# Kernel tuning notes

Measured on AMD Instinct MI355X. Metric: run time of the kernel, lower is better.

The kernel has to match this reference:

```python
import math
import jax, jax.numpy as jnp
import numpy as np

NUM_BUCKETS = 32
MAX_DISTANCE = 128
N_HEADS = 16
D_KV = 64


def _relative_position_bucket(rel_pos, num_buckets=NUM_BUCKETS, max_distance=MAX_DISTANCE):
    # bidirectional=True branch of T5's bucketing
    num_buckets = num_buckets // 2
    rel_buckets = (rel_pos > 0).astype(jnp.int32) * num_buckets
    rel_pos = jnp.abs(rel_pos)
    max_exact = num_buckets // 2
    is_small = rel_pos < max_exact
    # safe log (values < max_exact are masked out by is_small)
    rp_f = jnp.maximum(rel_pos, 1).astype(jnp.float32)
    rel_if_large = max_exact + (
        jnp.log(rp_f / max_exact) / math.log(max_distance / max_exact) * (num_buckets - max_exact)
    ).astype(jnp.int32)
    rel_if_large = jnp.minimum(rel_if_large, num_buckets - 1)
    return rel_buckets + jnp.where(is_small, rel_pos, rel_if_large)


def compute_bias(rel_bias_table, q_len, k_len):
    ctx = jnp.arange(q_len)[:, None]
    mem = jnp.arange(k_len)[None, :]
    buckets = _relative_position_bucket(mem - ctx)  # [q, k]
    values = rel_bias_table[buckets]                # [q, k, h]
    return jnp.transpose(values, (2, 0, 1))[None]   # [1, h, q, k]


def setup_inputs() -> dict:
    key = jax.random.key(0)
    k1, k2, k3, k4 = jax.random.split(key, 4)
    d_model = 1024
    return {
        "hidden_states": jax.random.normal(k1, (2, 2048, d_model), jnp.float32),
        "w_qkv": jax.random.normal(k2, (d_model, 3 * N_HEADS * D_KV), jnp.float32) * (d_model ** -0.5),
        "w_o": jax.random.normal(k3, (N_HEADS * D_KV, d_model), jnp.float32) * ((N_HEADS * D_KV) ** -0.5),
        "rel_bias_table": jax.random.normal(k4, (NUM_BUCKETS, N_HEADS), jnp.float32),
    }


def reference(hidden_states, w_qkv, w_o, rel_bias_table):
    b, s, _ = hidden_states.shape
    inner = N_HEADS * D_KV
    qkv = hidden_states @ w_qkv                         # [b, s, 3*inner]
    q, k, v = jnp.split(qkv, [inner, 2 * inner], axis=-1)
    def to_bhsd(x):
        return jnp.transpose(x.reshape(b, s, N_HEADS, D_KV), (0, 2, 1, 3))
    q, k, v = to_bhsd(q), to_bhsd(k), to_bhsd(v)
    scores = jnp.einsum("bhqd,bhkd->bhqk", q, k)        # no 1/sqrt(d) scaling in T5
    position_bias = compute_bias(rel_bias_table, s, s)  # [1, h, q, k]
    scores = scores + position_bias
    attn = jax.nn.softmax(scores.astype(jnp.float32), axis=-1).astype(scores.dtype)
    out = jnp.einsum("bhqk,bhkd->bhqd", attn, v)
    out = jnp.transpose(out, (0, 2, 1, 3)).reshape(b, s, inner)
    attn_output = out @ w_o
    return attn_output, position_bias
```

## Files before the change

kernel.cpp:

```cpp
#include <hip/hip_runtime.h>
#include <hip/hip_bf16.h>
#include <cstdint>
#include <cstddef>

#define S_LEN 2048
#define NH 16
#define DKV 64
#define BATCH 2
#define DMODEL 1024

typedef _Float16 half_t;
typedef __attribute__((ext_vector_type(4))) _Float16 halfx4;
typedef __attribute__((ext_vector_type(8))) _Float16 half8;
typedef __attribute__((ext_vector_type(4))) float floatx4;

__device__ __forceinline__ void load_lds16(const half_t* g, half_t* l) {
  __builtin_amdgcn_global_load_lds((const __attribute__((address_space(1))) void*)g,
                                   (__attribute__((address_space(3))) void*)l, 16, 0, 0);
}

__device__ __forceinline__ int t5_bucket(int delta) {
  int base = (delta > 0) ? 16 : 0;
  int a = delta < 0 ? -delta : delta;
  int n;
  if (a < 8)       n = a;
  else if (a < 12) n = 8;
  else if (a < 16) n = 9;
  else if (a < 23) n = 10;
  else if (a < 32) n = 11;
  else if (a < 46) n = 12;
  else if (a < 64) n = 13;
  else if (a < 91) n = 14;
  else             n = 15;
  return base + n;
}

__global__ __launch_bounds__(256) void bias_kernel(const float* __restrict__ table,
                                                   float* __restrict__ out) {
  int h = blockIdx.x >> 11;
  int q = blockIdx.x & (S_LEN - 1);
  __shared__ float tb[32];
  if (threadIdx.x < 32) tb[threadIdx.x] = table[threadIdx.x * NH + h];
  __syncthreads();
  float* dst = out + (size_t)blockIdx.x * S_LEN;
  int k0 = threadIdx.x * 4;
#pragma unroll
  for (int half = 0; half < 2; half++) {
    int k = k0 + half * 1024;
    float4 v;
    v.x = tb[t5_bucket((k + 0) - q)];
    v.y = tb[t5_bucket((k + 1) - q)];
    v.z = tb[t5_bucket((k + 2) - q)];
    v.w = tb[t5_bucket((k + 3) - q)];
    *(float4*)(dst + k) = v;
  }
}

__global__ __launch_bounds__(256) void cast_f2h(const float* __restrict__ in,
                                                half_t* __restrict__ out) {
  int i = blockIdx.x * 256 + threadIdx.x;
  float4 v = ((const float4*)in)[i];
  halfx4 h;
  h[0] = (half_t)v.x; h[1] = (half_t)v.y; h[2] = (half_t)v.z; h[3] = (half_t)v.w;
  ((halfx4*)out)[i] = h;
}

__global__ __launch_bounds__(256) void transpose_cast(const float* __restrict__ in,
                                                      half_t* __restrict__ out,
                                                      int R, int C) {
  __shared__ float t[32][33];
  int lr = threadIdx.x >> 3;
  int lc = (threadIdx.x & 7) * 4;
  int r0 = blockIdx.y * 32, c0 = blockIdx.x * 32;
  float4 v = *(const float4*)(in + (size_t)(r0 + lr) * C + c0 + lc);
  t[lr][lc + 0] = v.x; t[lr][lc + 1] = v.y; t[lr][lc + 2] = v.z; t[lr][lc + 3] = v.w;
  __syncthreads();
  halfx4 hv;
#pragma unroll
  for (int u = 0; u < 4; u++) hv[u] = (half_t)t[lc + u][lr];
  *(halfx4*)(out + (size_t)(c0 + lr) * R + r0 + lc) = hv;
}

template <int MODE>
__global__ __launch_bounds__(256) void hgemm128(const half_t* __restrict__ A,
                                                const half_t* __restrict__ Bt,
                                                float* __restrict__ C,
                                                half_t* __restrict__ Qo,
                                                half_t* __restrict__ Ko,
                                                half_t* __restrict__ Vto,
                                                int M, int N, int K) {
  __shared__ half_t Asl[8 * 512];
  __shared__ half_t Bsl[8 * 512];

  const int tid = threadIdx.x;
  const int w = tid >> 6;
  const int lane = tid & 63;
  const int l15 = lane & 15;
  const int quad = lane >> 4;
  const int wm = w >> 1, wn = w & 1;
  const int m0 = blockIdx.y * 128;
  const int n0 = blockIdx.x * 128;

  floatx4 acc[4][4];
#pragma unroll
  for (int i = 0; i < 4; i++)
#pragma unroll
    for (int j = 0; j < 4; j++) acc[i][j] = (floatx4){0.f, 0.f, 0.f, 0.f};

  const half_t* ga0 = A + (size_t)(m0 + (2 * w + 0) * 16 + l15) * K + quad * 8;
  const half_t* ga1 = A + (size_t)(m0 + (2 * w + 1) * 16 + l15) * K + quad * 8;
  const half_t* gb0 = Bt + (size_t)(n0 + (2 * w + 0) * 16 + l15) * K + quad * 8;
  const half_t* gb1 = Bt + (size_t)(n0 + (2 * w + 1) * 16 + l15) * K + quad * 8;
  half_t* la0 = &Asl[(2 * w + 0) * 512];
  half_t* la1 = &Asl[(2 * w + 1) * 512];
  half_t* lb0 = &Bsl[(2 * w + 0) * 512];
  half_t* lb1 = &Bsl[(2 * w + 1) * 512];

  for (int k0 = 0; k0 < K; k0 += 32) {
    __syncthreads();
    load_lds16(ga0 + k0, la0);
    load_lds16(ga1 + k0, la1);
    load_lds16(gb0 + k0, lb0);
    load_lds16(gb1 + k0, lb1);
    __syncthreads();

    half8 af[4], bf[4];
#pragma unroll
    for (int i = 0; i < 4; i++) af[i] = *(half8*)&Asl[(wm * 4 + i) * 512 + lane * 8];
#pragma unroll
    for (int j = 0; j < 4; j++) bf[j] = *(half8*)&Bsl[(wn * 4 + j) * 512 + lane * 8];
#pragma unroll
    for (int i = 0; i < 4; i++)
#pragma unroll
      for (int j = 0; j < 4; j++)
        acc[i][j] = __builtin_amdgcn_mfma_f32_16x16x32_f16(af[i], bf[j], acc[i][j], 0, 0, 0);
  }

  const int rowbase = m0 + wm * 64;
  const int colbase = n0 + wn * 64;
  if (MODE == 0) {
#pragma unroll
    for (int i = 0; i < 4; i++)
#pragma unroll
      for (int j = 0; j < 4; j++)
#pragma unroll
        for (int r = 0; r < 4; r++)
          C[(size_t)(rowbase + i * 16 + quad * 4 + r) * N + colbase + j * 16 + l15] =
              acc[i][j][r];
  } else {
    const int which = colbase >> 10;
    const int h = (colbase & 1023) >> 6;
    const int b = rowbase >> 11;
    const int s0 = rowbase & (S_LEN - 1);
    if (which < 2) {
      half_t* base = ((which == 0) ? Qo : Ko) + (size_t)(b * NH + h) * S_LEN * DKV;
#pragma unroll
      for (int i = 0; i < 4; i++)
#pragma unroll
        for (int j = 0; j < 4; j++)
#pragma unroll
          for (int r = 0; r < 4; r++)
            base[(size_t)(s0 + i * 16 + quad * 4 + r) * DKV + j * 16 + l15] =
                (half_t)acc[i][j][r];
    } else {
      half_t* base = Vto + (size_t)(b * NH + h) * DKV * S_LEN;
#pragma unroll
      for (int i = 0; i < 4; i++)
#pragma unroll
        for (int j = 0; j < 4; j++)
#pragma unroll
          for (int r = 0; r < 4; r++)
            base[(size_t)(j * 16 + l15) * S_LEN + s0 + i * 16 + quad * 4 + r] =
                (half_t)acc[i][j][r];
    }
  }
}

__global__ __launch_bounds__(256) void attn_mfma(const half_t* __restrict__ Q,
                                                 const half_t* __restrict__ K,
                                                 const half_t* __restrict__ Vt,
                                                 const float* __restrict__ table,
                                                 half_t* __restrict__ X) {
  __shared__ half_t Ks[64 * 64];
  __shared__ half_t Vts[64 * 64];
  __shared__ half_t Ps[64 * 68];
  __shared__ float tb[32];

  const int tid = threadIdx.x;
  const int w = tid >> 6;
  const int lane = tid & 63;
  const int l15 = lane & 15;
  const int quad = lane >> 4;
  const int bh = blockIdx.y;
  const int h = bh & (NH - 1);
  const int b = bh >> 4;
  const int q0 = blockIdx.x * 64;

  if (tid < 32) tb[tid] = table[tid * NH + h];

  half8 qf[2];
#pragma unroll
  for (int ks = 0; ks < 2; ks++)
    qf[ks] = *(const half8*)(Q + ((size_t)bh * S_LEN + q0 + w * 16 + l15) * DKV +
                             ks * 32 + quad * 8);

  floatx4 o[4];
  float m[4], l[4];
#pragma unroll
  for (int r = 0; r < 4; r++) { m[r] = -1e30f; l[r] = 0.0f; }
#pragma unroll
  for (int nb = 0; nb < 4; nb++) o[nb] = (floatx4){0.f, 0.f, 0.f, 0.f};

  const int jr = tid >> 2;
  const int ub = (tid & 3) * 2;

  for (int kc = 0; kc < S_LEN; kc += 64) {
    __syncthreads();
    {
      const half_t* Kg = K + ((size_t)bh * S_LEN + kc + jr) * DKV + ub * 8;
      const half_t* Vg = Vt + ((size_t)bh * DKV + jr) * S_LEN + kc + ub * 8;
      half8 k0v = *(const half8*)(Kg);
      half8 k1v = *(const half8*)(Kg + 8);
      half8 v0v = *(const half8*)(Vg);
      half8 v1v = *(const half8*)(Vg + 8);
      int sw = jr & 7;
      *(half8*)&Ks[jr * 64 + ((ub + 0) ^ sw) * 8] = k0v;
      *(half8*)&Ks[jr * 64 + ((ub + 1) ^ sw) * 8] = k1v;
      *(half8*)&Vts[jr * 64 + ((ub + 0) ^ sw) * 8] = v0v;
      *(half8*)&Vts[jr * 64 + ((ub + 1) ^ sw) * 8] = v1v;
    }
    __syncthreads();

    floatx4 s[4];
#pragma unroll
    for (int nb = 0; nb < 4; nb++) {
      s[nb] = (floatx4){0.f, 0.f, 0.f, 0.f};
      int key = nb * 16 + l15;
      int sw = key & 7;
#pragma unroll
      for (int ks = 0; ks < 2; ks++) {
        half8 bf = *(half8*)&Ks[key * 64 + ((ks * 4 + quad) ^ sw) * 8];
        s[nb] = __builtin_amdgcn_mfma_f32_16x16x32_f16(qf[ks], bf, s[nb], 0, 0, 0);
      }
    }

    float al[4];
#pragma unroll
    for (int r = 0; r < 4; r++) {
      int qabs = q0 + w * 16 + quad * 4 + r;
      float sv[4];
#pragma unroll
      for (int nb = 0; nb < 4; nb++)
        sv[nb] = s[nb][r] + tb[t5_bucket((kc + nb * 16 + l15) - qabs)];
      float cm = fmaxf(fmaxf(sv[0], sv[1]), fmaxf(sv[2], sv[3]));
#pragma unroll
      for (int msk = 1; msk <= 8; msk <<= 1) cm = fmaxf(cm, __shfl_xor(cm, msk));
      float mn = fmaxf(m[r], cm);
      al[r] = __expf(m[r] - mn);
      m[r] = mn;
      float psum = 0.0f;
#pragma unroll
      for (int nb = 0; nb < 4; nb++) {
        float p = __expf(sv[nb] - mn);
        psum += p;
        Ps[(w * 16 + quad * 4 + r) * 68 + nb * 16 + l15] = (half_t)p;
      }
#pragma unroll
      for (int msk = 1; msk <= 8; msk <<= 1) psum += __shfl_xor(psum, msk);
      l[r] = l[r] * al[r] + psum;
#pragma unroll
      for (int nb = 0; nb < 4; nb++) o[nb][r] *= al[r];
    }

    half8 af[2];
#pragma unroll
    for (int ks = 0; ks < 2; ks++)
      af[ks] = *(half8*)&Ps[(w * 16 + l15) * 68 + ks * 32 + quad * 8];
#pragma unroll
    for (int nb = 0; nb < 4; nb++) {
      int dd = nb * 16 + l15;
      int sw = dd & 7;
#pragma unroll
      for (int ks = 0; ks < 2; ks++) {
        half8 bf = *(half8*)&Vts[dd * 64 + ((ks * 4 + quad) ^ sw) * 8];
        o[nb] = __builtin_amdgcn_mfma_f32_16x16x32_f16(af[ks], bf, o[nb], 0, 0, 0);
      }
    }
  }

#pragma unroll
  for (int r = 0; r < 4; r++) {
    int q = q0 + w * 16 + quad * 4 + r;
    float inv = 1.0f / l[r];
    half_t* dst = X + (size_t)(b * S_LEN + q) * DMODEL + h * DKV;
#pragma unroll
    for (int nb = 0; nb < 4; nb++) dst[nb * 16 + l15] = (half_t)(o[nb][r] * inv);
  }
}

extern "C" void kernel_launch(void* const* d_in, const int* in_sizes, int n_in,
                              void* d_out, int out_size, void* d_ws, size_t ws_size,
                              hipStream_t stream) {
  const float* hidden = (const float*)d_in[0];
  const float* w_qkv = (const float*)d_in[1];
  const float* w_o = (const float*)d_in[2];
  const float* table = (const float*)d_in[3];

  float* attn_out = (float*)d_out;
  float* bias_out = (float*)d_out + 4194304;

  half_t* Ah  = (half_t*)d_ws;
  half_t* Wqt = Ah + 4194304;
  half_t* Wot = Wqt + 3145728;
  half_t* Qh  = Wot + 1048576;
  half_t* Kh  = Qh + 4194304;
  half_t* Vth = Kh + 4194304;
  half_t* Xh  = Vth + 4194304;

  cast_f2h<<<4096, 256, 0, stream>>>(hidden, Ah);
  transpose_cast<<<dim3(3072 / 32, 1024 / 32), 256, 0, stream>>>(w_qkv, Wqt, 1024, 3072);
  transpose_cast<<<dim3(1024 / 32, 1024 / 32), 256, 0, stream>>>(w_o, Wot, 1024, 1024);
  bias_kernel<<<NH * S_LEN, 256, 0, stream>>>(table, bias_out);

  hgemm128<1><<<dim3(3072 / 128, 4096 / 128), 256, 0, stream>>>(
      Ah, Wqt, nullptr, Qh, Kh, Vth, 4096, 3072, 1024);

  attn_mfma<<<dim3(S_LEN / 64, BATCH * NH), 256, 0, stream>>>(Qh, Kh, Vth, table, Xh);

  hgemm128<0><<<dim3(1024 / 128, 4096 / 128), 256, 0, stream>>>(
      Xh, Wot, attn_out, nullptr, nullptr, nullptr, 4096, 1024, 1024);
}
```

Measured before the change: 567.4 us.

## Precompute exp of relative bias and move V transpose to a separate kernel

```diff
diff --git a/kernel.cpp b/kernel.cpp
--- a/kernel.cpp
+++ b/kernel.cpp
@@ -81,13 +81,38 @@
   *(halfx4*)(out + (size_t)(c0 + lr) * R + r0 + lc) = hv;
 }
 
+__global__ __launch_bounds__(256) void vtrans(const half_t* __restrict__ V,
+                                              half_t* __restrict__ Vt) {
+  __shared__ half_t T[64 * 72];
+  const int bh = blockIdx.y;
+  const int s0 = blockIdx.x * 64;
+  const half_t* src = V + ((size_t)bh * S_LEN + s0) * DKV;
+  half_t* dst = Vt + (size_t)bh * DKV * S_LEN + s0;
+  const int sr = threadIdx.x >> 3;
+  const int dc = (threadIdx.x & 7) * 8;
+#pragma unroll
+  for (int p = 0; p < 2; p++) {
+    int s = sr + p * 32;
+    half8 v = *(const half8*)(src + (size_t)s * DKV + dc);
+#pragma unroll
+    for (int u = 0; u < 8; u++) T[(dc + u) * 72 + s] = v[u];
+  }
+  __syncthreads();
+#pragma unroll
+  for (int p = 0; p < 2; p++) {
+    int d = sr + p * 32;
+    half8 v = *(half8*)&T[d * 72 + dc];
+    *(half8*)(dst + (size_t)d * S_LEN + dc) = v;
+  }
+}
+
 template <int MODE>
 __global__ __launch_bounds__(256) void hgemm128(const half_t* __restrict__ A,
                                                 const half_t* __restrict__ Bt,
                                                 float* __restrict__ C,
                                                 half_t* __restrict__ Qo,
                                                 half_t* __restrict__ Ko,
-                                                half_t* __restrict__ Vto,
+                                                half_t* __restrict__ Vo,
                                                 int M, int N, int K) {
   __shared__ half_t Asl[8 * 512];
   __shared__ half_t Bsl[8 * 512];
@@ -152,27 +177,16 @@
     const int h = (colbase & 1023) >> 6;
     const int b = rowbase >> 11;
     const int s0 = rowbase & (S_LEN - 1);
-    if (which < 2) {
-      half_t* base = ((which == 0) ? Qo : Ko) + (size_t)(b * NH + h) * S_LEN * DKV;
-#pragma unroll
-      for (int i = 0; i < 4; i++)
-#pragma unroll
-        for (int j = 0; j < 4; j++)
-#pragma unroll
-          for (int r = 0; r < 4; r++)
-            base[(size_t)(s0 + i * 16 + quad * 4 + r) * DKV + j * 16 + l15] =
-                (half_t)acc[i][j][r];
-    } else {
-      half_t* base = Vto + (size_t)(b * NH + h) * DKV * S_LEN;
-#pragma unroll
-      for (int i = 0; i < 4; i++)
-#pragma unroll
-        for (int j = 0; j < 4; j++)
-#pragma unroll
-          for (int r = 0; r < 4; r++)
-            base[(size_t)(j * 16 + l15) * S_LEN + s0 + i * 16 + quad * 4 + r] =
-                (half_t)acc[i][j][r];
-    }
+    half_t* base = ((which == 0) ? Qo : (which == 1) ? Ko : Vo) +
+                   (size_t)(b * NH + h) * S_LEN * DKV;
+#pragma unroll
+    for (int i = 0; i < 4; i++)
+#pragma unroll
+      for (int j = 0; j < 4; j++)
+#pragma unroll
+        for (int r = 0; r < 4; r++)
+          base[(size_t)(s0 + i * 16 + quad * 4 + r) * DKV + j * 16 + l15] =
+              (half_t)acc[i][j][r];
   }
 }
 
@@ -185,6 +199,7 @@
   __shared__ half_t Vts[64 * 64];
   __shared__ half_t Ps[64 * 68];
   __shared__ float tb[32];
+  __shared__ float ebias[184];
 
   const int tid = threadIdx.x;
   const int w = tid >> 6;
@@ -197,6 +212,8 @@
   const int q0 = blockIdx.x * 64;
 
   if (tid < 32) tb[tid] = table[tid * NH + h];
+  __syncthreads();
+  if (tid < 183) ebias[tid] = __expf(tb[t5_bucket(tid - 91)]);
 
   half8 qf[2];
 #pragma unroll
@@ -248,11 +265,8 @@
 #pragma unroll
     for (int r = 0; r < 4; r++) {
       int qabs = q0 + w * 16 + quad * 4 + r;
-      float sv[4];
-#pragma unroll
-      for (int nb = 0; nb < 4; nb++)
-        sv[nb] = s[nb][r] + tb[t5_bucket((kc + nb * 16 + l15) - qabs)];
-      float cm = fmaxf(fmaxf(sv[0], sv[1]), fmaxf(sv[2], sv[3]));
+      int db = kc + l15 - qabs + 91;
+      float cm = fmaxf(fmaxf(s[0][r], s[1][r]), fmaxf(s[2][r], s[3][r]));
 #pragma unroll
       for (int msk = 1; msk <= 8; msk <<= 1) cm = fmaxf(cm, __shfl_xor(cm, msk));
       float mn = fmaxf(m[r], cm);
@@ -261,7 +275,9 @@
       float psum = 0.0f;
 #pragma unroll
       for (int nb = 0; nb < 4; nb++) {
-        float p = __expf(sv[nb] - mn);
+        int idx = db + nb * 16;
+        idx = idx < 0 ? 0 : (idx > 182 ? 182 : idx);
+        float p = __expf(s[nb][r] - mn) * ebias[idx];
         psum += p;
         Ps[(w * 16 + quad * 4 + r) * 68 + nb * 16 + l15] = (half_t)p;
       }
@@ -314,8 +330,9 @@
   half_t* Wot = Wqt + 3145728;
   half_t* Qh  = Wot + 1048576;
   half_t* Kh  = Qh + 4194304;
-  half_t* Vth = Kh + 4194304;
-  half_t* Xh  = Vth + 4194304;
+  half_t* Vh  = Kh + 4194304;
+  half_t* Xh  = Vh + 4194304;
+  half_t* Vth = Ah;
 
   cast_f2h<<<4096, 256, 0, stream>>>(hidden, Ah);
   transpose_cast<<<dim3(3072 / 32, 1024 / 32), 256, 0, stream>>>(w_qkv, Wqt, 1024, 3072);
@@ -323,7 +340,9 @@
   bias_kernel<<<NH * S_LEN, 256, 0, stream>>>(table, bias_out);
 
   hgemm128<1><<<dim3(3072 / 128, 4096 / 128), 256, 0, stream>>>(
-      Ah, Wqt, nullptr, Qh, Kh, Vth, 4096, 3072, 1024);
+      Ah, Wqt, nullptr, Qh, Kh, Vh, 4096, 3072, 1024);
+
+  vtrans<<<dim3(S_LEN / 64, BATCH * NH), 256, 0, stream>>>(Vh, Vth);
 
   attn_mfma<<<dim3(S_LEN / 64, BATCH * NH), 256, 0, stream>>>(Qh, Kh, Vth, table, Xh);
 
```

Result: faster. 538.1 us (-5.2%).
